# Optimization experiments

Measured on AMD Instinct MI355X. Metric: run time of the kernel, lower is better.

Reference implementation:

```python
import jax, jax.numpy as jnp
import numpy as np

B_GRAPHS = 256
N_PER = 512
N = B_GRAPHS * N_PER            # 131072 nodes
E = 1048576                     # edges (avg degree 8)
H = 64                          # hidden_dim
L = 3                           # num_layers
R = 128                         # rnn_dim
NODE_IN = 2
EDGE_IN = 2
OUT = 2
JK = L * H


def setup_inputs() -> dict:
    key = jax.random.key(0)
    ks = jax.random.split(key, 40)
    # intra-graph random edges
    g = jax.random.randint(ks[0], (E,), 0, B_GRAPHS)
    src = g * N_PER + jax.random.randint(ks[1], (E,), 0, N_PER)
    dst = g * N_PER + jax.random.randint(ks[2], (E,), 0, N_PER)
    edge_index = jnp.stack([src, dst]).astype(jnp.int64)
    batch = jnp.repeat(jnp.arange(B_GRAPHS, dtype=jnp.int64), N_PER)

    p = lambda k, shp: jax.random.normal(k, shp, jnp.float32) * 0.1
    return dict(
        x=jax.random.normal(ks[3], (N, NODE_IN), jnp.float32),
        edge_attr=jax.random.normal(ks[4], (E, EDGE_IN), jnp.float32),
        node_W=p(ks[5], (NODE_IN, H)), node_b=p(ks[6], (H,)),
        edgeemb_W=p(ks[7], (EDGE_IN, H)), edgeemb_b=p(ks[8], (H,)),
        gat_W=p(ks[9], (L, H, H)), gat_Wedge=p(ks[10], (L, H, H)),
        gat_att_src=p(ks[11], (L, H)), gat_att_dst=p(ks[12], (L, H)),
        gat_att_edge=p(ks[13], (L, H)), gat_b=p(ks[14], (L, H)),
        gru_wih_f=p(ks[15], (3 * R, JK)), gru_whh_f=p(ks[16], (3 * R, R)),
        gru_bih_f=p(ks[17], (3 * R,)), gru_bhh_f=p(ks[18], (3 * R,)),
        gru_wih_b=p(ks[19], (3 * R, JK)), gru_whh_b=p(ks[20], (3 * R, R)),
        gru_bih_b=p(ks[21], (3 * R,)), gru_bhh_b=p(ks[22], (3 * R,)),
        head_W1=p(ks[23], (2 * R, 64)), head_b1=p(ks[24], (64,)),
        head_W2=p(ks[25], (64, OUT)), head_b2=p(ks[26], (OUT,)),
        edge_index=edge_index, batch=batch,
    )


def _gru_dir(xs, wih, whh, bih, bhh):
    # xs: [T, B, F] -> outputs [T, B, R]  (PyTorch GRU cell equations)
    gx = xs @ wih.T + bih  # precompute input gates [T, B, 3R]
    h0 = jnp.zeros((xs.shape[1], R), xs.dtype)

    def step(h, g):
        gh = h @ whh.T + bhh
        r = jax.nn.sigmoid(g[..., :R] + gh[..., :R])
        z = jax.nn.sigmoid(g[..., R:2 * R] + gh[..., R:2 * R])
        n = jnp.tanh(g[..., 2 * R:] + r * gh[..., 2 * R:])
        hn = (1.0 - z) * n + z * h
        return hn, hn

    _, ys = jax.lax.scan(step, h0, gx)
    return ys


def _forward(x, edge_attr, node_W, node_b, edgeemb_W, edgeemb_b,
             gat_W, gat_Wedge, gat_att_src, gat_att_dst, gat_att_edge, gat_b,
             gru_wih_f, gru_whh_f, gru_bih_f, gru_bhh_f,
             gru_wih_b, gru_whh_b, gru_bih_b, gru_bhh_b,
             head_W1, head_b1, head_W2, head_b2, edge_index, batch):
    src, dst = edge_index[0], edge_index[1]
    h = x @ node_W + node_b                     # [N, H]
    e = edge_attr @ edgeemb_W + edgeemb_b       # [E, H]

    # PyG GATConv default add_self_loops=True, fill_value='mean':
    # self-loop edge feature = mean of incoming edge features per node
    ones = jnp.ones((E,), e.dtype)
    deg = jax.ops.segment_sum(ones, dst, num_segments=N)
    e_loop = jax.ops.segment_sum(e, dst, num_segments=N) / jnp.maximum(deg, 1.0)[:, None]
    ar = jnp.arange(N, dtype=src.dtype)
    srcF = jnp.concatenate([src, ar])
    dstF = jnp.concatenate([dst, ar])
    eF = jnp.concatenate([e, e_loop], axis=0)   # [E+N, H]

    outs = []
    for l in range(L):
        xp = h @ gat_W[l]                                   # [N, H]
        a_s = xp @ gat_att_src[l]                           # [N]
        a_d = xp @ gat_att_dst[l]                           # [N]
        a_e = (eF @ gat_Wedge[l]) @ gat_att_edge[l]         # [E+N]
        alpha = jax.nn.leaky_relu(a_s[srcF] + a_d[dstF] + a_e, 0.2)
        m = jax.ops.segment_max(alpha, dstF, num_segments=N)
        ex = jnp.exp(alpha - m[dstF])
        den = jax.ops.segment_sum(ex, dstF, num_segments=N)
        w = ex / den[dstF]                                  # segment softmax
        agg = jax.ops.segment_sum(w[:, None] * xp[srcF], dstF, num_segments=N) + gat_b[l]
        h = jax.nn.leaky_relu(agg, 0.01)                    # F.leaky_relu default slope
        outs.append(h)

    h_jk = jnp.concatenate(outs, axis=-1)                   # [N, JK]
    # to_dense_batch: sorted equal-size graphs -> dense reshape, mask all True
    dense = h_jk.reshape(B_GRAPHS, N_PER, JK)
    xs = dense.transpose(1, 0, 2)                           # [T, B, JK]
    yf = _gru_dir(xs, gru_wih_f, gru_whh_f, gru_bih_f, gru_bhh_f)
    yb = _gru_dir(xs[::-1], gru_wih_b, gru_whh_b, gru_bih_b, gru_bhh_b)[::-1]
    rnn_out = jnp.concatenate([yf, yb], axis=-1).transpose(1, 0, 2)  # [B, T, 2R]
    out = jax.nn.relu(rnn_out @ head_W1 + head_b1) @ head_W2 + head_b2
    return out.reshape(N, OUT)                              # out[mask], mask full


def reference(x, edge_attr, node_W, node_b, edgeemb_W, edgeemb_b,
              gat_W, gat_Wedge, gat_att_src, gat_att_dst, gat_att_edge, gat_b,
              gru_wih_f, gru_whh_f, gru_bih_f, gru_bhh_f,
              gru_wih_b, gru_whh_b, gru_bih_b, gru_bhh_b,
              head_W1, head_b1, head_W2, head_b2, edge_index, batch):
    return _forward(x, edge_attr, node_W, node_b, edgeemb_W, edgeemb_b,
                    gat_W, gat_Wedge, gat_att_src, gat_att_dst, gat_att_edge, gat_b,
                    gru_wih_f, gru_whh_f, gru_bih_f, gru_bhh_f,
                    gru_wih_b, gru_whh_b, gru_bih_b, gru_bhh_b,
                    head_W1, head_b1, head_W2, head_b2, edge_index, batch)
```

## Files before the change

### kernel.cpp

```cpp
#include <hip/hip_runtime.h>
#include <cstdint>
#include <cstddef>

typedef _Float16 half_t;
typedef _Float16 half8 __attribute__((ext_vector_type(8)));
typedef float f32x4 __attribute__((ext_vector_type(4)));

constexpr int NN = 131072;
constexpr int NE = 1048576;
constexpr int NPER = 512;

#define DEVINL __device__ __forceinline__

DEVINL float sigm_(float x){ float e = __expf(-x); return __builtin_amdgcn_rcpf(1.f+e); }
DEVINL float tanh_(float x){
  x = fminf(15.f, fmaxf(-15.f, x));
  float e = __expf(-2.f*x);
  return (1.f-e)*__builtin_amdgcn_rcpf(1.f+e);
}

#define LDS_BARRIER() asm volatile("s_waitcnt lgkmcnt(0)\ns_barrier" ::: "memory")


__global__ void const_kernel(const float* __restrict__ gatWe,
                             const float* __restrict__ attE, const float* __restrict__ eW,
                             const float* __restrict__ eb, float* __restrict__ cc){
  int l = blockIdx.x, k = threadIdx.x;
  const float* Wel = gatWe + l*4096;
  float s3=0.f;
  for (int j=0;j<64;j++) s3 += Wel[k*64+j]*attE[l*64+j];
  float c0 = eW[k]*s3, c1 = eW[64+k]*s3, cb = eb[k]*s3;
  for (int off=1; off<64; off<<=1){
    c0 += __shfl_xor(c0,off); c1 += __shfl_xor(c1,off); cb += __shfl_xor(cb,off);
  }
  if (k==0){ cc[l]=c0; cc[3+l]=c1; cc[6+l]=cb; }
}

__global__ void prep_pack(const float* __restrict__ wih_f, const float* __restrict__ wih_b,
                          const float* __restrict__ head_W1, const float* __restrict__ gat_W,
                          const float* __restrict__ bih_f, const float* __restrict__ bih_b,
                          const float* __restrict__ whh_f, const float* __restrict__ whh_b,
                          half_t* __restrict__ BcombT, half_t* __restrict__ W1T,
                          half_t* __restrict__ BTgat, float* __restrict__ bias_comb,
                          half_t* __restrict__ whh16){
  int gid = blockIdx.x*256 + threadIdx.x;
  if (gid < 147456){
    int j = gid/192, k = gid%192;
    float v = (j<384)? wih_f[j*192+k] : wih_b[(j-384)*192+k];
    BcombT[gid] = (half_t)v;
  } else if (gid < 163840){
    int i = gid - 147456;
    int n = i>>8, k = i&255;
    W1T[i] = (half_t)head_W1[k*64+n];
  } else if (gid < 176128){
    int i = gid - 163840;
    int l = i>>12, r = i&4095;
    int n = r>>6, k = r&63;
    BTgat[i] = (half_t)gat_W[l*4096 + k*64 + n];
  } else if (gid < 176896){
    int i = gid - 176128;
    int j = (i<384)? i : i-384;
    bias_comb[i] = (i<384)? bih_f[j] : bih_b[j];
  } else if (gid < 275200){
    int i = gid - 176896;
    float v = (i<49152)? whh_f[i] : whh_b[i-49152];
    whh16[i] = (half_t)v;
  }
}

__global__ void bias_fold(const float* __restrict__ bhh_f, const float* __restrict__ bhh_b,
                          float* __restrict__ bias_comb){
  int i = threadIdx.x + blockIdx.x*256;
  if (i < 256)      bias_comb[i]       += bhh_f[i];
  else if (i < 512) bias_comb[i+128]   += bhh_b[i-256];
}

__global__ __launch_bounds__(256) void embed_kernel(const float* __restrict__ x,
                            const float* __restrict__ nW, const float* __restrict__ nb,
                            half_t* __restrict__ h){
  int gid = blockIdx.x*256 + threadIdx.x;
  int n = gid>>6, j = gid&63;
  float v = x[2*n]*nW[j] + x[2*n+1]*nW[64+j] + nb[j];
  h[(size_t)n*64+j] = (half_t)v;
}

__global__ __launch_bounds__(256) void deg_count(const int* __restrict__ ei,
                          int* __restrict__ deg, int* __restrict__ tmp){
  int e = blockIdx.x*256 + threadIdx.x;
  int dt = ei[NE+e];
  tmp[e] = atomicAdd(&deg[dt],1);
}

__global__ __launch_bounds__(256) void scan1(const int* __restrict__ deg, int* __restrict__ rowstart,
                      int* __restrict__ bsum){
  __shared__ int sc[256];
  int b=blockIdx.x, t=threadIdx.x, i=b*256+t;
  int v=deg[i]; sc[t]=v; __syncthreads();
  for (int off=1; off<256; off<<=1){
    int tv = (t>=off)? sc[t-off] : 0;
    __syncthreads(); sc[t]+=tv; __syncthreads();
  }
  rowstart[i]=sc[t]-v;
  if (t==255) bsum[b]=sc[255];
}
__global__ void scan2(int* __restrict__ bsum){
  __shared__ int sc[512];
  int t=threadIdx.x; int v=bsum[t]; sc[t]=v; __syncthreads();
  for (int off=1; off<512; off<<=1){
    int tv = (t>=off)? sc[t-off] : 0;
    __syncthreads(); sc[t]+=tv; __syncthreads();
  }
  bsum[t]=sc[t]-v;
}
__global__ __launch_bounds__(256) void scan3(int* __restrict__ rowstart, const int* __restrict__ bsum){
  int b=blockIdx.x, t=threadIdx.x, i=b*256+t;
  rowstart[i]+=bsum[b];
}

__global__ __launch_bounds__(256) void fill2(const int* __restrict__ ei, const float* __restrict__ ea,
                      const int* __restrict__ rowstart, const int* __restrict__ tmp,
                      int4* __restrict__ rec){
  int e = blockIdx.x*256 + threadIdx.x;
  int dt = ei[NE+e];
  int slot = rowstart[dt] + tmp[e];
  int4 r;
  r.x = ei[e];
  r.y = __float_as_int(ea[2*e]);
  r.z = __float_as_int(ea[2*e+1]);
  r.w = dt;
  rec[slot] = r;
}

__global__ __launch_bounds__(256) void means_kernel(const int* __restrict__ deg, const int* __restrict__ rowstart,
                         const int4* __restrict__ rec, float2* __restrict__ m01){
  int n = blockIdx.x*256 + threadIdx.x;
  int st = rowstart[n], cnt = deg[n];
  float s0=0.f, s1=0.f;
  for (int i=0;i<cnt;i++){
    int4 r = rec[st+i];
    s0 += __int_as_float(r.y);
    s1 += __int_as_float(r.z);
  }
  float inv = 1.f/(float)max(cnt,1);
  float2 m; m.x = s0*inv; m.y = s1*inv;
  m01[n] = m;
}

__global__ __launch_bounds__(256) void gemm_xp(const half_t* __restrict__ A, int lda,
                        const half_t* __restrict__ BT,
                        const float* __restrict__ attS, const float* __restrict__ attD,
                        half_t* __restrict__ xp, float* __restrict__ a_s, float* __restrict__ a_d){
  __shared__ half_t As[128*32];
  __shared__ half_t Bs[64*32];
  const int tid = threadIdx.x, m0 = blockIdx.x*128;
  const int w = tid>>6, lane = tid&63;
  const int lm = lane&15, quad = lane>>4;
  const int wm0 = w*32;
  f32x4 acc[2][4] = {};
  for (int k0=0;k0<64;k0+=32){
    {
      const int c0 = tid*2;
      #pragma unroll
      for (int u=0;u<2;u++){
        int c=c0+u; int row=c>>2; int off=(c&3)*8;
        *(half8*)(&As[row*32+off]) = *(const half8*)(&A[(size_t)(m0+row)*lda + k0 + off]);
      }
      int c=tid; int row=c>>2; int off=(c&3)*8;
      *(half8*)(&Bs[row*32+off]) = *(const half8*)(&BT[(size_t)row*64 + k0 + off]);
    }
    __syncthreads();
    half8 af[2], bf[4];
    #pragma unroll
    for (int nt=0;nt<4;nt++) bf[nt] = *(const half8*)(&Bs[(nt*16+lm)*32 + quad*8]);
    #pragma unroll
    for (int mt=0;mt<2;mt++) af[mt] = *(const half8*)(&As[(wm0+mt*16+lm)*32 + quad*8]);
    #pragma unroll
    for (int mt=0;mt<2;mt++)
      #pragma unroll
      for (int nt=0;nt<4;nt++)
        acc[mt][nt] = __builtin_amdgcn_mfma_f32_16x16x32_f16(af[mt], bf[nt], acc[mt][nt], 0,0,0);
    __syncthreads();
  }
  float vsv[4], vdv[4];
  #pragma unroll
  for (int nt=0;nt<4;nt++){ vsv[nt]=attS[nt*16+lm]; vdv[nt]=attD[nt*16+lm]; }
  #pragma unroll
  for (int mt=0;mt<2;mt++)
   #pragma unroll
   for (int r=0;r<4;r++){
    int m = m0+wm0+mt*16+quad*4+r;
    float ps=0.f, pd=0.f;
    #pragma unroll
    for (int nt=0;nt<4;nt++){
      float v = acc[mt][nt][r];
      xp[(size_t)m*64 + nt*16+lm] = (half_t)v;
      ps += v*vsv[nt]; pd += v*vdv[nt];
    }
    ps += __shfl_xor(ps,1); ps += __shfl_xor(ps,2); ps += __shfl_xor(ps,4); ps += __shfl_xor(ps,8);
    pd += __shfl_xor(pd,1); pd += __shfl_xor(pd,2); pd += __shfl_xor(pd,4); pd += __shfl_xor(pd,8);
    if (lm==0){ a_s[m]=ps; a_d[m]=pd; }
  }
}

__global__ __launch_bounds__(256) void edge_w(const int4* __restrict__ rec,
                       const float* __restrict__ a_s, const float* __restrict__ a_d,
                       const float* __restrict__ cc, int l, int2* __restrict__ sw){
  int s = blockIdx.x*256 + threadIdx.x;
  int4 r = rec[s];
  float al = a_s[r.x] + a_d[r.w]
           + __int_as_float(r.y)*cc[l] + __int_as_float(r.z)*cc[3+l] + cc[6+l];
  al = al>0.f? al : 0.2f*al;
  int2 o; o.x = r.x; o.y = __float_as_int(__expf(al));
  sw[s] = o;
}

constexpr int SWCAP = 1536;
__global__ __launch_bounds__(512,4) void agg_lds(const int* __restrict__ rowstart, const int* __restrict__ deg,
                          const int2* __restrict__ sw,
                          const float* __restrict__ a_s, const float* __restrict__ a_d,
                          const float2* __restrict__ m01, const float* __restrict__ cc, int l,
                          const half_t* __restrict__ xp, const float* __restrict__ bias,
                          half_t* __restrict__ hjk){
  __shared__ half_t xs[512*64];
  __shared__ int2  swl[SWCAP];
  const int g = blockIdx.x >> 2;
  const int sub = blockIdx.x & 3;
  const int tid = threadIdx.x;
  const int nbase = g*512 + sub*128;
  const int segst = rowstart[nbase];
  const int segend = rowstart[nbase+127] + deg[nbase+127];
  const int segcnt = segend - segst;
  {
    const half8* srcp = (const half8*)(xp + (size_t)g*32768);
    half8* dstp = (half8*)xs;
    #pragma unroll
    for (int i=0;i<8;i++)
      dstp[tid + i*512] = srcp[tid + i*512];
    int scap = segcnt < SWCAP ? segcnt : SWCAP;
    for (int i=tid; i<scap; i+=512)
      swl[i] = sw[segst+i];
  }
  __syncthreads();
  const int w = tid>>6, lane = tid&63;
  const float bv = bias[lane];
  const float c0=cc[l], c1=cc[3+l], cb=cc[6+l];
  const int nb2 = nbase + w*16;
  for (int i=0;i<16;i++){
    int n = nb2 + i;
    int st = rowstart[n] - segst, cnt = deg[n];
    float acc=0.f, den=0.f;
    if (cnt>0){
      if (st + cnt <= SWCAP){
        int cA = cnt>>1, cB = cnt-cA;
        int2 pB = swl[st+cA];
        float xvB = (float)xs[(pB.x&511)*64 + lane];
        int2 pA = pB; float xvA = 0.f;
        if (cA>0){ pA = swl[st]; xvA = (float)xs[(pA.x&511)*64 + lane]; }
        for (int k=0;k<cB;k++){
          int2 pBn = pB; float xvBn=0.f;
          if (k+1<cB){ pBn = swl[st+cA+k+1]; xvBn = (float)xs[(pBn.x&511)*64 + lane]; }
          int2 pAn = pA; float xvAn=0.f;
          if (k+1<cA){ pAn = swl[st+k+1]; xvAn = (float)xs[(pAn.x&511)*64 + lane]; }
          float wB = __int_as_float(pB.y); den += wB; acc += wB*xvB;
          pB = pBn; xvB = xvBn;
          if (k<cA){ float wA = __int_as_float(pA.y); den += wA; acc += wA*xvA; }
          pA = pAn; xvA = xvAn;
        }
      } else {
        int2 p = sw[segst+st];
        float xv = (float)xs[(p.x&511)*64 + lane];
        for (int k=0;k<cnt;k++){
          int2 pn = p; float xvn=0.f;
          if (k+1<cnt){
            pn = sw[segst+st+k+1];
            xvn = (float)xs[(pn.x&511)*64 + lane];
          }
          float ww = __int_as_float(p.y);
          den += ww;
          acc += ww*xv;
          p = pn; xv = xvn;
        }
      }
    }
    float2 m = m01[n];
    float ael = cnt? (m.x*c0 + m.y*c1 + cb) : 0.f;
    float asl = a_s[n] + a_d[n] + ael;
    asl = asl>0.f? asl : 0.2f*asl;
    float wsf = __expf(asl);
    den += wsf;
    acc += wsf*(float)xs[(n&511)*64 + lane];
    float v = acc/den + bv;
    v = v>0.f? v : 0.01f*v;
    hjk[(size_t)n*192 + l*64 + lane] = (half_t)v;
  }
}

__global__ __launch_bounds__(256) void gemm_head(const half_t* __restrict__ A,
                        const half_t* __restrict__ W1T, const float* __restrict__ b1,
                        const float* __restrict__ W2, const float* __restrict__ b2,
                        float* __restrict__ out){
  __shared__ half_t As[128*32];
  __shared__ half_t Bs[64*32];
  const int tid = threadIdx.x, m0 = blockIdx.x*128;
  const int w = tid>>6, lane = tid&63;
  const int lm = lane&15, quad = lane>>4;
  const int wm0 = w*32;
  f32x4 acc[2][4] = {};
  for (int k0=0;k0<256;k0+=32){
    {
      const int c0 = tid*2;
      #pragma unroll
      for (int u=0;u<2;u++){
        int c=c0+u; int row=c>>2; int off=(c&3)*8;
        *(half8*)(&As[row*32+off]) = *(const half8*)(&A[(size_t)(m0+row)*256 + k0 + off]);
      }
      int c=tid; int row=c>>2; int off=(c&3)*8;
      *(half8*)(&Bs[row*32+off]) = *(const half8*)(&W1T[(size_t)row*256 + k0 + off]);
    }
    __syncthreads();
    half8 af[2], bf[4];
    #pragma unroll
    for (int nt=0;nt<4;nt++) bf[nt] = *(const half8*)(&Bs[(nt*16+lm)*32 + quad*8]);
    #pragma unroll
    for (int mt=0;mt<2;mt++) af[mt] = *(const half8*)(&As[(wm0+mt*16+lm)*32 + quad*8]);
    #pragma unroll
    for (int mt=0;mt<2;mt++)
      #pragma unroll
      for (int nt=0;nt<4;nt++)
        acc[mt][nt] = __builtin_amdgcn_mfma_f32_16x16x32_f16(af[mt], bf[nt], acc[mt][nt], 0,0,0);
    __syncthreads();
  }
  float b1v[4], w20[4], w21[4];
  #pragma unroll
  for (int nt=0;nt<4;nt++){
    int n = nt*16+lm;
    b1v[nt]=b1[n]; w20[nt]=W2[n*2]; w21[nt]=W2[n*2+1];
  }
  float b20=b2[0], b21=b2[1];
  #pragma unroll
  for (int mt=0;mt<2;mt++)
   #pragma unroll
   for (int r=0;r<4;r++){
    int m = m0+wm0+mt*16+quad*4+r;
    float p0=0.f, p1=0.f;
    #pragma unroll
    for (int nt=0;nt<4;nt++){
      float v = acc[mt][nt][r] + b1v[nt];
      v = v>0.f? v : 0.f;
      p0 += v*w20[nt]; p1 += v*w21[nt];
    }
    p0 += __shfl_xor(p0,1); p0 += __shfl_xor(p0,2); p0 += __shfl_xor(p0,4); p0 += __shfl_xor(p0,8);
    p1 += __shfl_xor(p1,1); p1 += __shfl_xor(p1,2); p1 += __shfl_xor(p1,4); p1 += __shfl_xor(p1,8);
    if (lm==0){
      out[(size_t)m*2]   = p0 + b20;
      out[(size_t)m*2+1] = p1 + b21;
    }
  }
}

__global__ __launch_bounds__(512,1) void gru_fused(
    const half_t* __restrict__ whh16, const float* __restrict__ bhh_f, const float* __restrict__ bhh_b,
    const half_t* __restrict__ gxf, const half_t* __restrict__ gxb,
    float* __restrict__ hstate, half_t* __restrict__ y, int c, int gruBlocks,
    const half_t* __restrict__ hjk, const half_t* __restrict__ BcombT, const float* __restrict__ biasc,
    half_t* __restrict__ gxf_n, half_t* __restrict__ gxb_n, int s0f, int s0b){
  __shared__ __align__(16) char SMEM[16384];
  const int bid = blockIdx.x;
  const int tid = threadIdx.x;
  if (bid < gruBlocks){
    __builtin_amdgcn_s_setprio(1);
    auto& H = *(half_t (*)[2][16][132])SMEM;
    half_t* slab0 = (half_t*)(SMEM + 8448);
    half_t* slab1 = (half_t*)(SMEM + 8448 + 3072);

    const int d = bid >> 6, gblk = bid & 63;
    const half_t* __restrict__ gx = d ? gxb : gxf;
    const float* bhh = d ? bhh_b : bhh_f;
    const int w = tid >> 6, lane = tid & 63;
    const int l15 = lane & 15, quad = lane >> 4;
    const int unit = w*16 + l15;

    half8 bf[3][4];
    float bhn = bhh[256 + unit];
    {
      const half_t* wbase = whh16 + (size_t)d*49152;
      #pragma unroll
      for (int g=0; g<3; g++){
        const half_t* wp = wbase + (size_t)(g*128 + unit)*128;
        #pragma unroll
        for (int kk=0; kk<4; kk++)
          bf[g][kk] = *(const half8*)(wp + kk*32 + quad*8);
      }
    }

    float hreg = hstate[((size_t)d*256 + gblk*4 + quad)*128 + unit];

    const bool loader = (w >= 4 && w < 7);
    const int jsl = d ? -384 : 384;
    int idx8 = 0;
    const half_t* srcp = nullptr;
    if (loader){
      int idx = (w-4)*64 + lane;
      int g_loc = idx/48, o = idx - g_loc*48;
      idx8 = idx*8;
      int j0 = d ? 127 : 0;
      srcp = gx + ((size_t)(gblk*4 + g_loc)*128 + j0)*384 + o*8;
    }

    const int cgg = tid >> 6;
    const int cpart = (tid & 63)*2;
    const int pos0 = d ? (511 - c*128) : (c*128);
    const int ystep = d ? -256 : 256;
    half_t* yptr = y + ((size_t)(gblk*4 + cgg)*512 + pos0)*256 + d*128 + cpart;

    for (int i=tid; i<2112; i+=512) ((uint*)SMEM)[i] = 0;
    LDS_BARRIER();
    H[0][quad*4][unit] = (half_t)hreg;
    half8 lvA, lvB;
    if (loader){
      lvA = *(const half8*)srcp; srcp += jsl;
      *(half8*)(slab0 + idx8) = lvA;
      lvB = *(const half8*)srcp; srcp += jsl;
    }
    LDS_BARRIER();

    auto stepf = [&](const half_t* cs, half_t* ns, int rd, int wr2,
                     half8& lvI, half8& lvW, bool pfi, bool pfw, bool cp){
      if (loader && pfi){ lvI = *(const half8*)srcp; srcp += jsl; }
      if (cp && tid < 256){
        uint hv = *(const uint*)&H[rd][cgg*4][cpart];
        *(uint*)yptr = hv;
        yptr += ystep;
      }
      float g0 = (float)cs[quad*384 + unit];
      float g1 = (float)cs[quad*384 + 128 + unit];
      float g2 = (float)cs[quad*384 + 256 + unit];
      half8 af[4] = {};
      if ((l15 & 3) == 0){
        #pragma unroll
        for (int kk=0; kk<4; kk++)
          af[kk] = *(const half8*)&H[rd][l15][kk*32 + quad*8];
      }
      f32x4 P[3] = {};
      #pragma unroll
      for (int kk=0; kk<4; kk++)
        #pragma unroll
        for (int g=0; g<3; g++)
          P[g] = __builtin_amdgcn_mfma_f32_16x16x32_f16(af[kk], bf[g][kk], P[g], 0,0,0);
      float rr = sigm_(g0 + P[0][0]);
      float zz = sigm_(g1 + P[1][0]);
      float nn = tanh_(g2 + rr*(P[2][0] + bhn));
      float hn = nn + zz*(hreg - nn);
      hreg = hn;
      H[wr2][quad*4][unit] = (half_t)hn;
      if (loader && pfw) *(half8*)(ns + idx8) = lvW;
      LDS_BARRIER();
    };

    stepf(slab0, slab1, 0,1, lvA, lvB, true,  true,  false);
    stepf(slab1, slab0, 1,0, lvB, lvA, true,  true,  true);
    for (int it=1; it<63; it++){
      stepf(slab0, slab1, 0,1, lvA, lvB, true, true, true);
      stepf(slab1, slab0, 1,0, lvB, lvA, true, true, true);
    }
    stepf(slab0, slab1, 0,1, lvA, lvB, false, true,  true);
    stepf(slab1, slab0, 1,0, lvB, lvA, false, false, true);
    if (tid < 256){
      uint hv = *(const uint*)&H[0][cgg*4][cpart];
      *(uint*)yptr = hv;
    }
    __builtin_amdgcn_s_setprio(0);
    hstate[((size_t)d*256 + gblk*4 + quad)*128 + unit] = hreg;
  } else {
    half_t* As = (half_t*)SMEM;
    half_t* Bs = (half_t*)(SMEM + 8192);
    const int gb = bid - gruBlocks;
    const int bx = gb & 255, by = gb >> 8;
    const int m0 = bx*128;
    const bool back = by >= 3;
    const int n0 = (back ? by-3 : by)*128;
    const int step0 = back ? s0b : s0f;
    half_t* C = back ? gxb_n : gxf_n;
    const half_t* BTh = BcombT + (back ? (size_t)384*192 : 0);
    const float* bh = biasc + (back ? 384 : 0);
    const int w = tid>>6, lane = tid&63;
    const int lm = lane&15, quad = lane>>4;
    const int wm0 = (w>>2)*64, wn0 = (w&3)*32;
    f32x4 acc[4][2] = {};
    for (int k0=0; k0<192; k0+=32){
      {
        int cidx = tid; int row = cidx>>2; int off = (cidx&3)*8;
        int m = m0+row;
        size_t arow = (size_t)(m>>7)*512 + step0 + (m&127);
        *(half8*)(&As[row*32+off]) = *(const half8*)(&hjk[arow*192 + k0 + off]);
        *(half8*)(&Bs[row*32+off]) = *(const half8*)(&BTh[(size_t)(n0+row)*192 + k0 + off]);
      }
      __syncthreads();
      half8 af[4], bfr[2];
      #pragma unroll
      for (int nt=0;nt<2;nt++) bfr[nt] = *(const half8*)(&Bs[(wn0+nt*16+lm)*32 + quad*8]);
      #pragma unroll
      for (int mt=0;mt<4;mt++) af[mt] = *(const half8*)(&As[(wm0+mt*16+lm)*32 + quad*8]);
      #pragma unroll
      for (int mt=0;mt<4;mt++)
        #pragma unroll
        for (int nt=0;nt<2;nt++)
          acc[mt][nt] = __builtin_amdgcn_mfma_f32_16x16x32_f16(af[mt], bfr[nt], acc[mt][nt], 0,0,0);
      __syncthreads();
    }
    #pragma unroll
    for (int mt=0;mt<4;mt++)
     #pragma unroll
     for (int nt=0;nt<2;nt++)
      #pragma unroll
      for (int r=0;r<4;r++){
        int m = m0+wm0+mt*16+quad*4+r;
        int n = n0+wn0+nt*16+lm;
        float v = acc[mt][nt][r] + bh[n];
        C[(size_t)m*384 + n] = (half_t)v;
      }
  }
}

extern "C" void kernel_launch(void* const* d_in, const int* in_sizes, int n_in,
                              void* d_out, int out_size, void* d_ws, size_t ws_size,
                              hipStream_t stream) {
  const float* x       = (const float*)d_in[0];
  const float* ea      = (const float*)d_in[1];
  const float* node_W  = (const float*)d_in[2];
  const float* node_b  = (const float*)d_in[3];
  const float* eW      = (const float*)d_in[4];
  const float* eb      = (const float*)d_in[5];
  const float* gat_W   = (const float*)d_in[6];
  const float* gat_We  = (const float*)d_in[7];
  const float* attS    = (const float*)d_in[8];
  const float* attD    = (const float*)d_in[9];
  const float* attE    = (const float*)d_in[10];
  const float* gat_b   = (const float*)d_in[11];
  const float* wih_f   = (const float*)d_in[12];
  const float* whh_f   = (const float*)d_in[13];
  const float* bih_f   = (const float*)d_in[14];
  const float* bhh_f   = (const float*)d_in[15];
  const float* wih_b   = (const float*)d_in[16];
  const float* whh_b   = (const float*)d_in[17];
  const float* bih_b   = (const float*)d_in[18];
  const float* bhh_b   = (const float*)d_in[19];
  const float* head_W1 = (const float*)d_in[20];
  const float* head_b1 = (const float*)d_in[21];
  const float* head_W2 = (const float*)d_in[22];
  const float* head_b2 = (const float*)d_in[23];
  const int*   ei      = (const int*)d_in[24];
  float* out = (float*)d_out;
  char* ws = (char*)d_ws;
  (void)in_sizes; (void)n_in; (void)out_size; (void)ws_size;

  size_t o = 0;
  auto alloc = [&](size_t bytes)->size_t{ size_t r=o; o += (bytes+255)&~(size_t)255; return r; };
  size_t o_cc     = alloc(16*4);
  size_t o_biasc  = alloc(768*4);
  size_t o_BcombT = alloc((size_t)768*192*2);
  size_t o_BTgat  = alloc((size_t)3*4096*2);
  size_t o_W1T    = alloc((size_t)64*256*2);
  size_t o_whh16  = alloc((size_t)2*49152*2);
  size_t o_hstate = alloc((size_t)2*256*128*4);
  size_t shared_base = o;

  size_t o_deg    = alloc((size_t)NN*4);
  size_t zero_end = o;
  size_t o_tmp    = alloc((size_t)NE*4);
  size_t o_rows   = alloc((size_t)NN*4);
  size_t o_bsum   = alloc(512*4);
  size_t o_rec    = alloc((size_t)NE*16);
  size_t o_sw     = alloc((size_t)NE*8);
  size_t o_m01    = alloc((size_t)NN*8);
  size_t o_as     = alloc((size_t)NN*4);
  size_t o_ad     = alloc((size_t)NN*4);
  size_t o_h      = alloc((size_t)NN*64*2);
  size_t o_xp     = alloc((size_t)NN*64*2);
  size_t gat_end  = o;
  size_t gat_size = gat_end - shared_base;

  const size_t GXC    = (size_t)256*128*384*2;
  const size_t HJK_SZ = (size_t)NN*192*2;
  size_t shared_sz = gat_size > 4*GXC ? gat_size : 4*GXC;
  size_t o_gx0f = shared_base;
  size_t o_gx0b = shared_base + GXC;
  size_t o_gx1f = shared_base + 2*GXC;
  size_t o_gx1b = shared_base + 3*GXC;
  size_t o_hjk = shared_base + shared_sz;
  size_t o_y   = o_hjk + HJK_SZ;

  int*    deg    = (int*)(ws+o_deg);
  int*    tmp    = (int*)(ws+o_tmp);
  int*    rows   = (int*)(ws+o_rows);
  int*    bsum   = (int*)(ws+o_bsum);
  int4*   rec    = (int4*)(ws+o_rec);
  int2*   sw     = (int2*)(ws+o_sw);
  float2* m01    = (float2*)(ws+o_m01);
  float*  a_s    = (float*)(ws+o_as);
  float*  a_d    = (float*)(ws+o_ad);
  float*  cc     = (float*)(ws+o_cc);
  float*  biasc  = (float*)(ws+o_biasc);
  half_t* h      = (half_t*)(ws+o_h);
  half_t* xp     = (half_t*)(ws+o_xp);
  half_t* hjk    = (half_t*)(ws+o_hjk);
  half_t* BcombT = (half_t*)(ws+o_BcombT);
  half_t* BTgat  = (half_t*)(ws+o_BTgat);
  half_t* W1T    = (half_t*)(ws+o_W1T);
  half_t* whh16  = (half_t*)(ws+o_whh16);
  float*  hstate = (float*)(ws+o_hstate);
  half_t* gxbuf[2][2] = {{(half_t*)(ws+o_gx0f), (half_t*)(ws+o_gx0b)},
                         {(half_t*)(ws+o_gx1f), (half_t*)(ws+o_gx1b)}};
  half_t* y      = (half_t*)(ws+o_y);

  hipMemsetAsync(ws+shared_base, 0, zero_end-shared_base, stream);
  hipMemsetAsync(ws+o_hstate, 0, (size_t)2*256*128*4, stream);

  const_kernel<<<3,64,0,stream>>>(gat_We, attE, eW, eb, cc);
  prep_pack<<<1075,256,0,stream>>>(wih_f, wih_b, head_W1, gat_W, bih_f, bih_b, whh_f, whh_b,
                                   BcombT, W1T, BTgat, biasc, whh16);
  bias_fold<<<2,256,0,stream>>>(bhh_f, bhh_b, biasc);
  embed_kernel<<<32768,256,0,stream>>>(x, node_W, node_b, h);
  deg_count<<<4096,256,0,stream>>>(ei, deg, tmp);
  scan1<<<512,256,0,stream>>>(deg, rows, bsum);
  scan2<<<1,512,0,stream>>>(bsum);
  scan3<<<512,256,0,stream>>>(rows, bsum);
  fill2<<<4096,256,0,stream>>>(ei, ea, rows, tmp, rec);
  means_kernel<<<512,256,0,stream>>>(deg, rows, rec, m01);

  for (int l=0;l<3;l++){
    const half_t* in = (l==0)? h : (hjk + (size_t)(l-1)*64);
    int lda = (l==0)? 64 : 192;
    gemm_xp<<<1024,256,0,stream>>>(in, lda, BTgat + (size_t)l*4096, attS + l*64, attD + l*64, xp, a_s, a_d);
    edge_w<<<4096,256,0,stream>>>(rec, a_s, a_d, cc, l, sw);
    agg_lds<<<1024,512,0,stream>>>(rows, deg, sw, a_s, a_d, m01, cc, l, xp, gat_b + l*64, hjk);
  }

  gru_fused<<<1536,512,0,stream>>>(whh16, bhh_f, bhh_b, gxbuf[0][0], gxbuf[0][1], hstate, y, 0, 0,
                                   hjk, BcombT, biasc, gxbuf[0][0], gxbuf[0][1], 0, 384);
  for (int c=0;c<4;c++){
    int buf = c&1, nbuf = (c+1)&1;
    int grid = 128 + (c<3 ? 1536 : 0);
    gru_fused<<<grid,512,0,stream>>>(whh16, bhh_f, bhh_b, gxbuf[buf][0], gxbuf[buf][1], hstate, y, c, 128,
                                     hjk, BcombT, biasc, gxbuf[nbuf][0], gxbuf[nbuf][1],
                                     (c+1)*128, (2-c)*128);
  }

  gemm_head<<<1024,256,0,stream>>>(y, W1T, head_b1, head_W2, head_b2, out);
}
```

Measured before the change: 824.1 us.

## Precompute self-loop weights in edge_w, stage per-node metadata in LDS, 4-way aggregation ILP

The self-loop attention weight for each node is now computed in extra blocks of edge_w and written to a new wsf buffer, so agg_lds no longer reads a_s, a_d, m01 and cc per node. agg_lds stages row start, degree and self weight for its 128 nodes in shared memory once, instead of each wave reading them from global memory. The neighbour accumulation loop now splits each node's edges into four interleaved streams instead of two, giving more independent LDS loads in flight. The cost is an extra global buffer and a larger edge_w grid, plus higher register pressure in agg_lds, which already runs under launch_bounds(512,4).

After: 770.8 us. 6.5% less time.

```diff
diff --git a/kernel.cpp b/kernel.cpp
--- a/kernel.cpp
+++ b/kernel.cpp
@@ -204,25 +204,39 @@
 
 __global__ __launch_bounds__(256) void edge_w(const int4* __restrict__ rec,
                        const float* __restrict__ a_s, const float* __restrict__ a_d,
-                       const float* __restrict__ cc, int l, int2* __restrict__ sw){
-  int s = blockIdx.x*256 + threadIdx.x;
-  int4 r = rec[s];
-  float al = a_s[r.x] + a_d[r.w]
-           + __int_as_float(r.y)*cc[l] + __int_as_float(r.z)*cc[3+l] + cc[6+l];
-  al = al>0.f? al : 0.2f*al;
-  int2 o; o.x = r.x; o.y = __float_as_int(__expf(al));
-  sw[s] = o;
+                       const float* __restrict__ cc, int l, int2* __restrict__ sw,
+                       const int* __restrict__ deg, const float2* __restrict__ m01,
+                       float* __restrict__ wsf){
+  int b = blockIdx.x;
+  if (b < 4096){
+    int s = b*256 + threadIdx.x;
+    int4 r = rec[s];
+    float al = a_s[r.x] + a_d[r.w]
+             + __int_as_float(r.y)*cc[l] + __int_as_float(r.z)*cc[3+l] + cc[6+l];
+    al = al>0.f? al : 0.2f*al;
+    int2 o; o.x = r.x; o.y = __float_as_int(__expf(al));
+    sw[s] = o;
+  } else {
+    int n = (b-4096)*256 + threadIdx.x;
+    int cnt = deg[n];
+    float2 m = m01[n];
+    float ael = cnt? (m.x*cc[l] + m.y*cc[3+l] + cc[6+l]) : 0.f;
+    float asl = a_s[n] + a_d[n] + ael;
+    asl = asl>0.f? asl : 0.2f*asl;
+    wsf[n] = __expf(asl);
+  }
 }
 
 constexpr int SWCAP = 1536;
 __global__ __launch_bounds__(512,4) void agg_lds(const int* __restrict__ rowstart, const int* __restrict__ deg,
-                          const int2* __restrict__ sw,
-                          const float* __restrict__ a_s, const float* __restrict__ a_d,
-                          const float2* __restrict__ m01, const float* __restrict__ cc, int l,
+                          const int2* __restrict__ sw, const float* __restrict__ wsf, int l,
                           const half_t* __restrict__ xp, const float* __restrict__ bias,
                           half_t* __restrict__ hjk){
   __shared__ half_t xs[512*64];
   __shared__ int2  swl[SWCAP];
+  __shared__ int   nst[128];
+  __shared__ int   ncnt[128];
+  __shared__ float nwsf[128];
   const int g = blockIdx.x >> 2;
   const int sub = blockIdx.x & 3;
   const int tid = threadIdx.x;
@@ -239,32 +253,45 @@
     int scap = segcnt < SWCAP ? segcnt : SWCAP;
     for (int i=tid; i<scap; i+=512)
       swl[i] = sw[segst+i];
+    if (tid < 128){
+      int n = nbase + tid;
+      nst[tid]  = rowstart[n] - segst;
+      ncnt[tid] = deg[n];
+      nwsf[tid] = wsf[n];
+    }
   }
   __syncthreads();
   const int w = tid>>6, lane = tid&63;
   const float bv = bias[lane];
-  const float c0=cc[l], c1=cc[3+l], cb=cc[6+l];
   const int nb2 = nbase + w*16;
   for (int i=0;i<16;i++){
-    int n = nb2 + i;
-    int st = rowstart[n] - segst, cnt = deg[n];
+    const int li = w*16 + i;
+    int st = nst[li], cnt = ncnt[li];
     float acc=0.f, den=0.f;
     if (cnt>0){
       if (st + cnt <= SWCAP){
-        int cA = cnt>>1, cB = cnt-cA;
-        int2 pB = swl[st+cA];
-        float xvB = (float)xs[(pB.x&511)*64 + lane];
-        int2 pA = pB; float xvA = 0.f;
-        if (cA>0){ pA = swl[st]; xvA = (float)xs[(pA.x&511)*64 + lane]; }
-        for (int k=0;k<cB;k++){
-          int2 pBn = pB; float xvBn=0.f;
-          if (k+1<cB){ pBn = swl[st+cA+k+1]; xvBn = (float)xs[(pBn.x&511)*64 + lane]; }
-          int2 pAn = pA; float xvAn=0.f;
-          if (k+1<cA){ pAn = swl[st+k+1]; xvAn = (float)xs[(pAn.x&511)*64 + lane]; }
-          float wB = __int_as_float(pB.y); den += wB; acc += wB*xvB;
-          pB = pBn; xvB = xvBn;
-          if (k<cA){ float wA = __int_as_float(pA.y); den += wA; acc += wA*xvA; }
-          pA = pAn; xvA = xvAn;
+        int q = cnt>>2, rem = cnt&3;
+        int L0=q+(rem>0), L1=q+(rem>1), L2=q+(rem>2), L3=q;
+        int s1v=L0, s2v=L0+L1, s3v=s2v+L2;
+        int2 p0={0,0},p1={0,0},p2={0,0},p3={0,0};
+        float x0v=0.f,x1v=0.f,x2v=0.f,x3v=0.f;
+        if (L0>0){ p0=swl[st];     x0v=(float)xs[(p0.x&511)*64+lane]; }
+        if (L1>0){ p1=swl[st+s1v]; x1v=(float)xs[(p1.x&511)*64+lane]; }
+        if (L2>0){ p2=swl[st+s2v]; x2v=(float)xs[(p2.x&511)*64+lane]; }
+        if (L3>0){ p3=swl[st+s3v]; x3v=(float)xs[(p3.x&511)*64+lane]; }
+        for (int k=0;k<L0;k++){
+          int2 n0=p0,n1=p1,n2=p2,n3=p3;
+          float y0=0.f,y1=0.f,y2=0.f,y3=0.f;
+          if (k+1<L0){ n0=swl[st+k+1];     y0=(float)xs[(n0.x&511)*64+lane]; }
+          if (k+1<L1){ n1=swl[st+s1v+k+1]; y1=(float)xs[(n1.x&511)*64+lane]; }
+          if (k+1<L2){ n2=swl[st+s2v+k+1]; y2=(float)xs[(n2.x&511)*64+lane]; }
+          if (k+1<L3){ n3=swl[st+s3v+k+1]; y3=(float)xs[(n3.x&511)*64+lane]; }
+          { float ww=__int_as_float(p0.y); den+=ww; acc+=ww*x0v; }
+          if (k<L1){ float ww=__int_as_float(p1.y); den+=ww; acc+=ww*x1v; }
+          if (k<L2){ float ww=__int_as_float(p2.y); den+=ww; acc+=ww*x2v; }
+          if (k<L3){ float ww=__int_as_float(p3.y); den+=ww; acc+=ww*x3v; }
+          p0=n0;p1=n1;p2=n2;p3=n3;
+          x0v=y0;x1v=y1;x2v=y2;x3v=y3;
         }
       } else {
         int2 p = sw[segst+st];
@@ -282,16 +309,12 @@
         }
       }
     }
-    float2 m = m01[n];
-    float ael = cnt? (m.x*c0 + m.y*c1 + cb) : 0.f;
-    float asl = a_s[n] + a_d[n] + ael;
-    asl = asl>0.f? asl : 0.2f*asl;
-    float wsf = __expf(asl);
-    den += wsf;
-    acc += wsf*(float)xs[(n&511)*64 + lane];
+    float wsfv = nwsf[li];
+    den += wsfv;
+    acc += wsfv*(float)xs[((nb2+i)&511)*64 + lane];
     float v = acc/den + bv;
     v = v>0.f? v : 0.01f*v;
-    hjk[(size_t)n*192 + l*64 + lane] = (half_t)v;
+    hjk[(size_t)(nb2+i)*192 + l*64 + lane] = (half_t)v;
   }
 }
 
@@ -575,6 +598,7 @@
   size_t o_m01    = alloc((size_t)NN*8);
   size_t o_as     = alloc((size_t)NN*4);
   size_t o_ad     = alloc((size_t)NN*4);
+  size_t o_wsf    = alloc((size_t)NN*4);
   size_t o_h      = alloc((size_t)NN*64*2);
   size_t o_xp     = alloc((size_t)NN*64*2);
   size_t gat_end  = o;
@@ -599,6 +623,7 @@
   float2* m01    = (float2*)(ws+o_m01);
   float*  a_s    = (float*)(ws+o_as);
   float*  a_d    = (float*)(ws+o_ad);
+  float*  wsf    = (float*)(ws+o_wsf);
   float*  cc     = (float*)(ws+o_cc);
   float*  biasc  = (float*)(ws+o_biasc);
   half_t* h      = (half_t*)(ws+o_h);
@@ -632,8 +657,8 @@
     const half_t* in = (l==0)? h : (hjk + (size_t)(l-1)*64);
     int lda = (l==0)? 64 : 192;
     gemm_xp<<<1024,256,0,stream>>>(in, lda, BTgat + (size_t)l*4096, attS + l*64, attD + l*64, xp, a_s, a_d);
-    edge_w<<<4096,256,0,stream>>>(rec, a_s, a_d, cc, l, sw);
-    agg_lds<<<1024,512,0,stream>>>(rows, deg, sw, a_s, a_d, m01, cc, l, xp, gat_b + l*64, hjk);
+    edge_w<<<4608,256,0,stream>>>(rec, a_s, a_d, cc, l, sw, deg, m01, wsf);
+    agg_lds<<<1024,512,0,stream>>>(rows, deg, sw, wsf, l, xp, gat_b + l*64, hjk);
   }
 
   gru_fused<<<1536,512,0,stream>>>(whh16, bhh_f, bhh_b, gxbuf[0][0], gxbuf[0][1], hstate, y, 0, 0,
```
